# Kernel optimization log

Measured on AMD Instinct MI355X. Metric: run time of the kernel, lower is better.

## Reference

```python
import jax, jax.numpy as jnp
import numpy as np

B, N, M = 4, 512, 8192
QUERY_DIM, INPUT_DIM = 512, 256
HEADS, DIM_HEAD = 8, 64
ATT_DIM = HEADS * DIM_HEAD  # 512


def setup_inputs() -> dict:
    key = jax.random.key(0)
    ks = jax.random.split(key, 6)
    x = jax.random.normal(ks[0], (B, N, QUERY_DIM), dtype=jnp.float32)
    context = jax.random.normal(ks[1], (B, M, INPUT_DIM), dtype=jnp.float32)
    # Linear weights stored as [in, out] for x @ W
    Wq = jax.random.normal(ks[2], (QUERY_DIM, ATT_DIM), dtype=jnp.float32) / np.sqrt(QUERY_DIM)
    Wkv = jax.random.normal(ks[3], (INPUT_DIM, 2 * ATT_DIM), dtype=jnp.float32) / np.sqrt(INPUT_DIM)
    Wo = jax.random.normal(ks[4], (ATT_DIM, QUERY_DIM), dtype=jnp.float32) / np.sqrt(ATT_DIM)
    bo = jax.random.normal(ks[5], (QUERY_DIM,), dtype=jnp.float32) * 0.01
    return {"x": x, "context": context, "Wq": Wq, "Wkv": Wkv, "Wo": Wo, "bo": bo}


def reference(x, context, Wq, Wkv, Wo, bo):
    scale = DIM_HEAD ** -0.5
    q = x @ Wq                      # [B, N, H*D]
    kv = context @ Wkv              # [B, M, 2*H*D]
    k, v = jnp.split(kv, 2, axis=-1)
    # split heads: b n (h d) -> b h n d
    q = q.reshape(B, N, HEADS, DIM_HEAD).transpose(0, 2, 1, 3)
    k = k.reshape(B, M, HEADS, DIM_HEAD).transpose(0, 2, 1, 3)
    v = v.reshape(B, M, HEADS, DIM_HEAD).transpose(0, 2, 1, 3)
    scores = jnp.einsum('bhid,bhjd->bhij', q, k) * scale  # [B, H, N, M]
    attn = jax.nn.softmax(scores, axis=-1)
    out = jnp.einsum('bhij,bhjd->bhid', attn, v)           # [B, H, N, D]
    out = out.transpose(0, 2, 1, 3).reshape(B, N, ATT_DIM)
    return out @ Wo + bo
```

## Files before the change

### kernel.cpp

```cpp
#include <hip/hip_runtime.h>
#include <hip/hip_bf16.h>
#include <cstdint>

#define NB 4
#define NQ 512
#define NM 8192
#define NH 8
#define DH 64

typedef short bf16x8s __attribute__((ext_vector_type(8)));
typedef float f32x4  __attribute__((ext_vector_type(4)));

static __device__ __forceinline__ short f2bs(float f) {
    unsigned u = __builtin_bit_cast(unsigned, f);
    return (short)(unsigned short)((u + 0x8000u) >> 16);
}
static __device__ __forceinline__ unsigned pk2(float a, float b) {
    unsigned au = __builtin_bit_cast(unsigned, a) + 0x8000u;
    unsigned bu = __builtin_bit_cast(unsigned, b) + 0x8000u;
    return __builtin_amdgcn_perm(bu, au, 0x07060302u);
}

__device__ __forceinline__ void proj32_body(
    const float* __restrict__ A, const float* __restrict__ W,
    float* __restrict__ C, const float* __restrict__ bias,
    int tm, int tn, char* smemraw)
{
    short* As = (short*)smemraw;
    short* Bs = As + 32 * 72;

    const int t = threadIdx.x;
    const int w = t >> 6, ln = t & 63;
    const int m16 = ln & 15, quad = ln >> 4;
    const int wm = w >> 1, wn = w & 1;

    const int ar = t >> 3, ac = (t & 7) << 3;
    const int bn = t & 63, bkh = (t >> 6) << 4;

    const float* Ap = A + (size_t)(tm * 32 + ar) * 512 + ac;
    const float* Bp = W + (size_t)bkh * 512 + tn * 64 + bn;

    f32x4 acc[2] = {};

    for (int k0 = 0; k0 < 512; k0 += 64) {
        float4 a0 = *(const float4*)(Ap + k0);
        float4 a1 = *(const float4*)(Ap + k0 + 4);
        float bv[16];
        #pragma unroll
        for (int kk = 0; kk < 16; ++kk)
            bv[kk] = Bp[(size_t)(k0 + kk) * 512];

        __syncthreads();
        {
            uint4 wa = { pk2(a0.x,a0.y), pk2(a0.z,a0.w), pk2(a1.x,a1.y), pk2(a1.z,a1.w) };
            *(uint4*)&As[ar * 72 + ac] = wa;
            uint4 v0 = { pk2(bv[0],bv[1]),  pk2(bv[2],bv[3]),   pk2(bv[4],bv[5]),   pk2(bv[6],bv[7]) };
            uint4 v1 = { pk2(bv[8],bv[9]),  pk2(bv[10],bv[11]), pk2(bv[12],bv[13]), pk2(bv[14],bv[15]) };
            *(uint4*)&Bs[bn * 72 + bkh]     = v0;
            *(uint4*)&Bs[bn * 72 + bkh + 8] = v1;
        }
        __syncthreads();

        #pragma unroll
        for (int ks = 0; ks < 2; ++ks) {
            bf16x8s af = *(const bf16x8s*)&As[(wm * 16 + m16) * 72 + ks * 32 + quad * 8];
            #pragma unroll
            for (int nt = 0; nt < 2; ++nt) {
                bf16x8s bf = *(const bf16x8s*)&Bs[(wn * 32 + nt * 16 + m16) * 72 + ks * 32 + quad * 8];
                acc[nt] = __builtin_amdgcn_mfma_f32_16x16x32_bf16(af, bf, acc[nt], 0, 0, 0);
            }
        }
    }

    const int row0 = tm * 32 + wm * 16 + quad * 4;
    const int col0 = tn * 64 + wn * 32;
    #pragma unroll
    for (int nt = 0; nt < 2; ++nt) {
        const int col = col0 + nt * 16 + m16;
        const float bb = bias ? bias[col] : 0.f;
        #pragma unroll
        for (int r = 0; r < 4; ++r)
            C[(size_t)(row0 + r) * 512 + col] = acc[nt][r] + bb;
    }
}

__device__ __forceinline__ void kv_body(
    const float* __restrict__ A, const float* __restrict__ Bw,
    short* __restrict__ Kf, short* __restrict__ Vf,
    int bid, char* smemraw)
{
    short* As = (short*)smemraw;
    short* Bs = As + 128 * 40;

    const int t  = threadIdx.x;
    const int tm = bid & 255, tn = bid >> 8;
    const int w  = t >> 6, ln = t & 63;
    const int m16 = ln & 15, quad = ln >> 4;
    const int wm = w & 1, wn = w >> 1;

    const int ar = t >> 3;
    const int ac = (t & 7) << 2;
    const int sb_n = t & 127, sb_kh = (t >> 7) << 4;

    const float* Abase = A  + (size_t)(tm * 128 + ar) * 256 + ac;
    const float* Bbase = Bw + (size_t)sb_kh * 1024 + tn * 128 + sb_n;

    f32x4 acc[4][4] = {};

    for (int k0 = 0; k0 < 256; k0 += 32) {
        float4 av[4];
        #pragma unroll
        for (int p = 0; p < 4; ++p)
            av[p] = *(const float4*)(Abase + (size_t)p * 32 * 256 + k0);
        float bv[16];
        #pragma unroll
        for (int kk = 0; kk < 16; ++kk)
            bv[kk] = Bbase[(size_t)(k0 + kk) * 1024];

        __syncthreads();
        #pragma unroll
        for (int p = 0; p < 4; ++p) {
            uint2 wv = { pk2(av[p].x, av[p].y), pk2(av[p].z, av[p].w) };
            *(uint2*)&As[(p * 32 + ar) * 40 + ac] = wv;
        }
        {
            uint4 v0 = { pk2(bv[0],bv[1]),  pk2(bv[2],bv[3]),   pk2(bv[4],bv[5]),   pk2(bv[6],bv[7]) };
            uint4 v1 = { pk2(bv[8],bv[9]),  pk2(bv[10],bv[11]), pk2(bv[12],bv[13]), pk2(bv[14],bv[15]) };
            *(uint4*)&Bs[sb_n * 40 + sb_kh]     = v0;
            *(uint4*)&Bs[sb_n * 40 + sb_kh + 8] = v1;
        }
        __syncthreads();

        bf16x8s af[4], bfr[4];
        #pragma unroll
        for (int i = 0; i < 4; ++i)
            af[i] = *(const bf16x8s*)&As[(wm * 64 + i * 16 + m16) * 40 + quad * 8];
        #pragma unroll
        for (int j = 0; j < 4; ++j)
            bfr[j] = *(const bf16x8s*)&Bs[(wn * 64 + j * 16 + m16) * 40 + quad * 8];
        #pragma unroll
        for (int i = 0; i < 4; ++i)
            #pragma unroll
            for (int j = 0; j < 4; ++j)
                acc[i][j] = __builtin_amdgcn_mfma_f32_16x16x32_bf16(af[i], bfr[j], acc[i][j], 0, 0, 0);
    }

    const int col0 = tn * 128 + wn * 64;
    const int row0 = tm * 128 + wm * 64;
    const int b    = row0 >> 13;
    const int mr0  = row0 & (NM - 1);

    if (col0 < 512) {
        const int h = col0 >> 6;
        short* Kp = Kf + (size_t)(b * NH + h) * (NM * DH);
        #pragma unroll
        for (int i = 0; i < 4; ++i)
            #pragma unroll
            for (int j = 0; j < 4; ++j) {
                const int d = j * 16 + m16;
                #pragma unroll
                for (int r = 0; r < 4; ++r) {
                    const int key = mr0 + i * 16 + quad * 4 + r;
                    const int idx = ((key >> 4) * 2 + (d >> 5)) * 512
                                  + (((d >> 3) & 3) * 16 + (key & 15)) * 8 + (d & 7);
                    Kp[idx] = f2bs(acc[i][j][r]);
                }
            }
    } else {
        const int h = (col0 - 512) >> 6;
        short* Vp = Vf + (size_t)(b * NH + h) * (NM * DH);
        #pragma unroll
        for (int i = 0; i < 4; ++i)
            #pragma unroll
            for (int j = 0; j < 4; ++j) {
                const int key0 = mr0 + i * 16 + quad * 4;
                const int idx = (j * 256 + (key0 >> 5)) * 512
                              + ((((key0 >> 3) & 3) * 16 + m16) * 8) + (key0 & 7);
                uint2 pk;
                pk.x = pk2(acc[i][j][0], acc[i][j][1]);
                pk.y = pk2(acc[i][j][2], acc[i][j][3]);
                *(uint2*)(Vp + idx) = pk;
            }
    }
}

__global__ __launch_bounds__(256) void gemm_kvq(
    const float* __restrict__ x,   const float* __restrict__ Wq, float* __restrict__ q,
    const float* __restrict__ ctx, const float* __restrict__ Wkv,
    short* __restrict__ Kf, short* __restrict__ Vf)
{
    __shared__ __align__(16) char smem[20480];
    if (blockIdx.x < 512)
        proj32_body(x, Wq, q, nullptr, (int)(blockIdx.x >> 3), (int)(blockIdx.x & 7), smem);
    else
        kv_body(ctx, Wkv, Kf, Vf, (int)(blockIdx.x - 512), smem);
}

__global__ __launch_bounds__(256) void gemm_proj32(
    const float* __restrict__ A, const float* __restrict__ W,
    float* __restrict__ C, const float* __restrict__ bias)
{
    __shared__ __align__(16) char smem[(32 + 64) * 72 * 2];
    proj32_body(A, W, C, bias, (int)(blockIdx.x >> 3), (int)(blockIdx.x & 7), smem);
}

__global__ __launch_bounds__(256) void attn_mfma(
    const float* __restrict__ Q,
    const short* __restrict__ Kfr,
    const short* __restrict__ Vfr,
    float* __restrict__ Og)
{
    __shared__ __align__(16) float Obuf[4 * 32 * 68];
    __shared__ float lbuf[4 * 32];

    const int bid = blockIdx.x;
    const int xcd = bid & 7, grp = bid >> 3;
    const int bh  = xcd * 4 + (grp & 3);
    const int qt  = grp >> 2;
    const int b   = bh >> 3, h = bh & 7;
    const int t   = threadIdx.x;
    const int w   = t >> 6, ln = t & 63;
    const int m16 = ln & 15, quad = ln >> 4;

    const short* Kbase = Kfr + (size_t)bh * (NM * DH);
    const short* Vbase = Vfr + (size_t)bh * (NM * DH);

    bf16x8s qf[2][2];
    #pragma unroll
    for (int mt = 0; mt < 2; ++mt) {
        const float* qrow = Q + ((size_t)(b * NQ + qt * 32 + mt * 16 + m16)) * 512 + h * 64;
        #pragma unroll
        for (int ks = 0; ks < 2; ++ks) {
            float4 x0 = *(const float4*)(qrow + ks * 32 + quad * 8);
            float4 x1 = *(const float4*)(qrow + ks * 32 + quad * 8 + 4);
            uint4 pkv = { pk2(x0.x * 0.125f, x0.y * 0.125f), pk2(x0.z * 0.125f, x0.w * 0.125f),
                          pk2(x1.x * 0.125f, x1.y * 0.125f), pk2(x1.z * 0.125f, x1.w * 0.125f) };
            qf[mt][ks] = *reinterpret_cast<bf16x8s*>(&pkv);
        }
    }

    f32x4 o[2][4] = {};
    float lpr[2] = {0.f, 0.f};

    const int srcLo = (((quad << 1) & 3) << 4) + m16;
    const int srcHi = ((((quad << 1) + 1) & 3) << 4) + m16;
    const bool ktHi = quad >= 2;

    bf16x8s kf[4][2];
    {
        const int kc = w * 64;
        #pragma unroll
        for (int nt = 0; nt < 4; ++nt)
            #pragma unroll
            for (int ks = 0; ks < 2; ++ks)
                kf[nt][ks] = *(const bf16x8s*)(Kbase + ((((kc >> 4) + nt) * 2 + ks) << 9) + ln * 8);
    }

    for (int it = 0; it < 32; ++it) {
        const int kc = it * 256 + w * 64;

        bf16x8s vf[4][2];
        #pragma unroll
        for (int dt = 0; dt < 4; ++dt)
            #pragma unroll
            for (int ks = 0; ks < 2; ++ks)
                vf[dt][ks] = *(const bf16x8s*)(Vbase + ((dt * 256 + (kc >> 5) + ks) << 9) + ln * 8);

        f32x4 st[2][4] = {};
        #pragma unroll
        for (int kt = 0; kt < 4; ++kt)
            #pragma unroll
            for (int mt = 0; mt < 2; ++mt) {
                st[mt][kt] = __builtin_amdgcn_mfma_f32_16x16x32_bf16(kf[kt][0], qf[mt][0], st[mt][kt], 0, 0, 0);
                st[mt][kt] = __builtin_amdgcn_mfma_f32_16x16x32_bf16(kf[kt][1], qf[mt][1], st[mt][kt], 0, 0, 0);
            }

        if (it + 1 < 32) {
            const int kn = (it + 1) * 256 + w * 64;
            #pragma unroll
            for (int nt = 0; nt < 4; ++nt)
                #pragma unroll
                for (int ks = 0; ks < 2; ++ks)
                    kf[nt][ks] = *(const bf16x8s*)(Kbase + ((((kn >> 4) + nt) * 2 + ks) << 9) + ln * 8);
        }

        unsigned pp[2][4][2];
        #pragma unroll
        for (int mt = 0; mt < 2; ++mt)
            #pragma unroll
            for (int kt = 0; kt < 4; ++kt) {
                const float p0 = __expf(st[mt][kt][0]);
                const float p1 = __expf(st[mt][kt][1]);
                const float p2 = __expf(st[mt][kt][2]);
                const float p3 = __expf(st[mt][kt][3]);
                lpr[mt] += (p0 + p1) + (p2 + p3);
                pp[mt][kt][0] = pk2(p0, p1);
                pp[mt][kt][1] = pk2(p2, p3);
            }

        #pragma unroll
        for (int mt = 0; mt < 2; ++mt)
            #pragma unroll
            for (int ks = 0; ks < 2; ++ks) {
                const unsigned a0 = __shfl(pp[mt][2 * ks][0], srcLo);
                const unsigned b0 = __shfl(pp[mt][2 * ks + 1][0], srcLo);
                const unsigned a1 = __shfl(pp[mt][2 * ks][1], srcLo);
                const unsigned b1 = __shfl(pp[mt][2 * ks + 1][1], srcLo);
                const unsigned a2 = __shfl(pp[mt][2 * ks][0], srcHi);
                const unsigned b2 = __shfl(pp[mt][2 * ks + 1][0], srcHi);
                const unsigned a3 = __shfl(pp[mt][2 * ks][1], srcHi);
                const unsigned b3 = __shfl(pp[mt][2 * ks + 1][1], srcHi);
                uint4 pb;
                pb.x = ktHi ? b0 : a0;
                pb.y = ktHi ? b1 : a1;
                pb.z = ktHi ? b2 : a2;
                pb.w = ktHi ? b3 : a3;
                bf16x8s pbv = *reinterpret_cast<bf16x8s*>(&pb);
                #pragma unroll
                for (int dt = 0; dt < 4; ++dt)
                    o[mt][dt] = __builtin_amdgcn_mfma_f32_16x16x32_bf16(vf[dt][ks], pbv, o[mt][dt], 0, 0, 0);
            }
    }

    float lf[2];
    #pragma unroll
    for (int mt = 0; mt < 2; ++mt) {
        float l = lpr[mt];
        l += __shfl_xor(l, 16);
        l += __shfl_xor(l, 32);
        lf[mt] = l;
    }

    #pragma unroll
    for (int mt = 0; mt < 2; ++mt)
        #pragma unroll
        for (int dt = 0; dt < 4; ++dt)
            *(f32x4*)&Obuf[(w * 32 + mt * 16 + m16) * 68 + dt * 16 + quad * 4] = o[mt][dt];
    if (quad == 0) {
        lbuf[w * 32 +      m16] = lf[0];
        lbuf[w * 32 + 16 + m16] = lf[1];
    }
    __syncthreads();
    {
        const int row = t >> 3, d0 = (t & 7) << 3;
        const float l = lbuf[row] + lbuf[32 + row] + lbuf[64 + row] + lbuf[96 + row];
        const float inv = 1.0f / l;
        float res[8];
        #pragma unroll
        for (int j = 0; j < 8; ++j) {
            float a = Obuf[(row) * 68 + d0 + j]
                    + Obuf[(32 + row) * 68 + d0 + j]
                    + Obuf[(64 + row) * 68 + d0 + j]
                    + Obuf[(96 + row) * 68 + d0 + j];
            res[j] = a * inv;
        }
        float* op = Og + ((size_t)(b * NQ + qt * 32 + row)) * 512 + h * 64 + d0;
        float4 r0 = {res[0], res[1], res[2], res[3]};
        float4 r1 = {res[4], res[5], res[6], res[7]};
        *(float4*)op = r0;
        *(float4*)(op + 4) = r1;
    }
}

extern "C" void kernel_launch(void* const* d_in, const int* in_sizes, int n_in,
                              void* d_out, int out_size, void* d_ws, size_t ws_size,
                              hipStream_t stream) {
    (void)in_sizes; (void)n_in; (void)out_size; (void)ws_size;

    const float* x   = (const float*)d_in[0];
    const float* ctx = (const float*)d_in[1];
    const float* Wq  = (const float*)d_in[2];
    const float* Wkv = (const float*)d_in[3];
    const float* Wo  = (const float*)d_in[4];
    const float* bo  = (const float*)d_in[5];
    float* out = (float*)d_out;

    float* ws    = (float*)d_ws;
    float* q     = ws;
    float* attno = q + (size_t)2048 * 512;
    short* Kf    = (short*)(attno + (size_t)2048 * 512);
    short* Vf    = Kf + (size_t)NB * NH * NM * DH;

    gemm_kvq<<<dim3(2560), dim3(256), 0, stream>>>(x, Wq, q, ctx, Wkv, Kf, Vf);

    attn_mfma<<<dim3(512), dim3(256), 0, stream>>>(q, Kf, Vf, attno);

    gemm_proj32<<<dim3(512), dim3(256), 0, stream>>>(attno, Wo, out, bo);
}
```

Before: 205.3 us.

## Pre-pack weights into MFMA fragment layout and offload softmax row sums to MFMA

Adds a prep kernel that converts Wq, Wo and Wkv to bf16 in MFMA B-fragment order, so the GEMMs load B fragments straight from global memory. This removes the strided fp32 loads, LDS staging and LDS reads for weights, and halves shared memory. In attention, exp is replaced by exp2 with log2e folded into the Q scale, and the row sum is computed by an extra MFMA against a ones vector instead of VALU adds and shuffles. The cost is one extra kernel launch and weight conversion work on every call.

```diff
diff --git a/kernel.cpp b/kernel.cpp
--- a/kernel.cpp
+++ b/kernel.cpp
@@ -21,13 +21,39 @@
     return __builtin_amdgcn_perm(bu, au, 0x07060302u);
 }
 
+#if __has_builtin(__builtin_amdgcn_exp2f)
+static __device__ __forceinline__ float fexp2(float x) { return __builtin_amdgcn_exp2f(x); }
+#else
+static __device__ __forceinline__ float fexp2(float x) { return exp2f(x); }
+#endif
+
+__global__ __launch_bounds__(256) void prep_weights(
+    const float* __restrict__ Wq, const float* __restrict__ Wo,
+    const float* __restrict__ Wkv,
+    short* __restrict__ Wqf, short* __restrict__ Wof, short* __restrict__ Wkvf)
+{
+    const int t = threadIdx.x;
+    const int w = t >> 6, ln = t & 63;
+    const int m16 = ln & 15, quad = ln >> 4;
+    int f = blockIdx.x * 4 + w;
+    const float* src; short* dst; int N, KS, n0, ks;
+    if (f < 512)       { src = Wq;  dst = Wqf;  N = 512;  KS = 16; n0 = f >> 4; ks = f & 15; }
+    else if (f < 1024) { f -= 512;  src = Wo;  dst = Wof;  N = 512;  KS = 16; n0 = f >> 4; ks = f & 15; }
+    else               { f -= 1024; src = Wkv; dst = Wkvf; N = 1024; KS = 8;  n0 = f >> 3; ks = f & 7; }
+    const float* sp = src + (size_t)(ks * 32 + quad * 8) * N + n0 * 16 + m16;
+    float v[8];
+    #pragma unroll
+    for (int j = 0; j < 8; ++j) v[j] = sp[(size_t)j * N];
+    uint4 pkv = { pk2(v[0],v[1]), pk2(v[2],v[3]), pk2(v[4],v[5]), pk2(v[6],v[7]) };
+    *(uint4*)(dst + ((size_t)(n0 * KS + ks) * 64 + ln) * 8) = pkv;
+}
+
 __device__ __forceinline__ void proj32_body(
-    const float* __restrict__ A, const float* __restrict__ W,
+    const float* __restrict__ A, const short* __restrict__ Wf,
     float* __restrict__ C, const float* __restrict__ bias,
     int tm, int tn, char* smemraw)
 {
     short* As = (short*)smemraw;
-    short* Bs = As + 32 * 72;
 
     const int t = threadIdx.x;
     const int w = t >> 6, ln = t & 63;
@@ -35,29 +61,26 @@
     const int wm = w >> 1, wn = w & 1;
 
     const int ar = t >> 3, ac = (t & 7) << 3;
-    const int bn = t & 63, bkh = (t >> 6) << 4;
 
     const float* Ap = A + (size_t)(tm * 32 + ar) * 512 + ac;
-    const float* Bp = W + (size_t)bkh * 512 + tn * 64 + bn;
 
     f32x4 acc[2] = {};
 
     for (int k0 = 0; k0 < 512; k0 += 64) {
         float4 a0 = *(const float4*)(Ap + k0);
         float4 a1 = *(const float4*)(Ap + k0 + 4);
-        float bv[16];
-        #pragma unroll
-        for (int kk = 0; kk < 16; ++kk)
-            bv[kk] = Bp[(size_t)(k0 + kk) * 512];
+        bf16x8s bfr[2][2];
+        #pragma unroll
+        for (int ks = 0; ks < 2; ++ks)
+            #pragma unroll
+            for (int nt = 0; nt < 2; ++nt)
+                bfr[ks][nt] = *(const bf16x8s*)(Wf +
+                    ((size_t)((tn * 4 + wn * 2 + nt) * 16 + (k0 >> 5) + ks) * 64 + ln) * 8);
 
         __syncthreads();
         {
             uint4 wa = { pk2(a0.x,a0.y), pk2(a0.z,a0.w), pk2(a1.x,a1.y), pk2(a1.z,a1.w) };
             *(uint4*)&As[ar * 72 + ac] = wa;
-            uint4 v0 = { pk2(bv[0],bv[1]),  pk2(bv[2],bv[3]),   pk2(bv[4],bv[5]),   pk2(bv[6],bv[7]) };
-            uint4 v1 = { pk2(bv[8],bv[9]),  pk2(bv[10],bv[11]), pk2(bv[12],bv[13]), pk2(bv[14],bv[15]) };
-            *(uint4*)&Bs[bn * 72 + bkh]     = v0;
-            *(uint4*)&Bs[bn * 72 + bkh + 8] = v1;
         }
         __syncthreads();
 
@@ -65,10 +88,8 @@
         for (int ks = 0; ks < 2; ++ks) {
             bf16x8s af = *(const bf16x8s*)&As[(wm * 16 + m16) * 72 + ks * 32 + quad * 8];
             #pragma unroll
-            for (int nt = 0; nt < 2; ++nt) {
-                bf16x8s bf = *(const bf16x8s*)&Bs[(wn * 32 + nt * 16 + m16) * 72 + ks * 32 + quad * 8];
-                acc[nt] = __builtin_amdgcn_mfma_f32_16x16x32_bf16(af, bf, acc[nt], 0, 0, 0);
-            }
+            for (int nt = 0; nt < 2; ++nt)
+                acc[nt] = __builtin_amdgcn_mfma_f32_16x16x32_bf16(af, bfr[ks][nt], acc[nt], 0, 0, 0);
         }
     }
 
@@ -85,12 +106,11 @@
 }
 
 __device__ __forceinline__ void kv_body(
-    const float* __restrict__ A, const float* __restrict__ Bw,
+    const float* __restrict__ A, const short* __restrict__ Wkvf,
     short* __restrict__ Kf, short* __restrict__ Vf,
     int bid, char* smemraw)
 {
     short* As = (short*)smemraw;
-    short* Bs = As + 128 * 40;
 
     const int t  = threadIdx.x;
     const int tm = bid & 255, tn = bid >> 8;
@@ -100,10 +120,8 @@
 
     const int ar = t >> 3;
     const int ac = (t & 7) << 2;
-    const int sb_n = t & 127, sb_kh = (t >> 7) << 4;
-
-    const float* Abase = A  + (size_t)(tm * 128 + ar) * 256 + ac;
-    const float* Bbase = Bw + (size_t)sb_kh * 1024 + tn * 128 + sb_n;
+
+    const float* Abase = A + (size_t)(tm * 128 + ar) * 256 + ac;
 
     f32x4 acc[4][4] = {};
 
@@ -112,10 +130,11 @@
         #pragma unroll
         for (int p = 0; p < 4; ++p)
             av[p] = *(const float4*)(Abase + (size_t)p * 32 * 256 + k0);
-        float bv[16];
-        #pragma unroll
-        for (int kk = 0; kk < 16; ++kk)
-            bv[kk] = Bbase[(size_t)(k0 + kk) * 1024];
+        bf16x8s bfr[4];
+        #pragma unroll
+        for (int j = 0; j < 4; ++j)
+            bfr[j] = *(const bf16x8s*)(Wkvf +
+                ((size_t)((tn * 8 + wn * 4 + j) * 8 + (k0 >> 5)) * 64 + ln) * 8);
 
         __syncthreads();
         #pragma unroll
@@ -123,21 +142,12 @@
             uint2 wv = { pk2(av[p].x, av[p].y), pk2(av[p].z, av[p].w) };
             *(uint2*)&As[(p * 32 + ar) * 40 + ac] = wv;
         }
-        {
-            uint4 v0 = { pk2(bv[0],bv[1]),  pk2(bv[2],bv[3]),   pk2(bv[4],bv[5]),   pk2(bv[6],bv[7]) };
-            uint4 v1 = { pk2(bv[8],bv[9]),  pk2(bv[10],bv[11]), pk2(bv[12],bv[13]), pk2(bv[14],bv[15]) };
-            *(uint4*)&Bs[sb_n * 40 + sb_kh]     = v0;
-            *(uint4*)&Bs[sb_n * 40 + sb_kh + 8] = v1;
-        }
         __syncthreads();
 
-        bf16x8s af[4], bfr[4];
+        bf16x8s af[4];
         #pragma unroll
         for (int i = 0; i < 4; ++i)
             af[i] = *(const bf16x8s*)&As[(wm * 64 + i * 16 + m16) * 40 + quad * 8];
-        #pragma unroll
-        for (int j = 0; j < 4; ++j)
-            bfr[j] = *(const bf16x8s*)&Bs[(wn * 64 + j * 16 + m16) * 40 + quad * 8];
         #pragma unroll
         for (int i = 0; i < 4; ++i)
             #pragma unroll
@@ -185,23 +195,23 @@
 }
 
 __global__ __launch_bounds__(256) void gemm_kvq(
-    const float* __restrict__ x,   const float* __restrict__ Wq, float* __restrict__ q,
-    const float* __restrict__ ctx, const float* __restrict__ Wkv,
+    const float* __restrict__ x,   const short* __restrict__ Wqf, float* __restrict__ q,
+    const float* __restrict__ ctx, const short* __restrict__ Wkvf,
     short* __restrict__ Kf, short* __restrict__ Vf)
 {
-    __shared__ __align__(16) char smem[20480];
+    __shared__ __align__(16) char smem[10240];
     if (blockIdx.x < 512)
-        proj32_body(x, Wq, q, nullptr, (int)(blockIdx.x >> 3), (int)(blockIdx.x & 7), smem);
+        proj32_body(x, Wqf, q, nullptr, (int)(blockIdx.x >> 3), (int)(blockIdx.x & 7), smem);
     else
-        kv_body(ctx, Wkv, Kf, Vf, (int)(blockIdx.x - 512), smem);
+        kv_body(ctx, Wkvf, Kf, Vf, (int)(blockIdx.x - 512), smem);
 }
 
 __global__ __launch_bounds__(256) void gemm_proj32(
-    const float* __restrict__ A, const float* __restrict__ W,
+    const float* __restrict__ A, const short* __restrict__ Wf,
     float* __restrict__ C, const float* __restrict__ bias)
 {
-    __shared__ __align__(16) char smem[(32 + 64) * 72 * 2];
-    proj32_body(A, W, C, bias, (int)(blockIdx.x >> 3), (int)(blockIdx.x & 7), smem);
+    __shared__ __align__(16) char smem[32 * 72 * 2];
+    proj32_body(A, Wf, C, bias, (int)(blockIdx.x >> 3), (int)(blockIdx.x & 7), smem);
 }
 
 __global__ __launch_bounds__(256) void attn_mfma(
@@ -225,6 +235,7 @@
     const short* Kbase = Kfr + (size_t)bh * (NM * DH);
     const short* Vbase = Vfr + (size_t)bh * (NM * DH);
 
+    const float qsc = 0.125f * 1.44269504f;
     bf16x8s qf[2][2];
     #pragma unroll
     for (int mt = 0; mt < 2; ++mt) {
@@ -233,14 +244,18 @@
         for (int ks = 0; ks < 2; ++ks) {
             float4 x0 = *(const float4*)(qrow + ks * 32 + quad * 8);
             float4 x1 = *(const float4*)(qrow + ks * 32 + quad * 8 + 4);
-            uint4 pkv = { pk2(x0.x * 0.125f, x0.y * 0.125f), pk2(x0.z * 0.125f, x0.w * 0.125f),
-                          pk2(x1.x * 0.125f, x1.y * 0.125f), pk2(x1.z * 0.125f, x1.w * 0.125f) };
+            uint4 pkv = { pk2(x0.x * qsc, x0.y * qsc), pk2(x0.z * qsc, x0.w * qsc),
+                          pk2(x1.x * qsc, x1.y * qsc), pk2(x1.z * qsc, x1.w * qsc) };
             qf[mt][ks] = *reinterpret_cast<bf16x8s*>(&pkv);
         }
     }
 
+    bf16x8s ones;
+    #pragma unroll
+    for (int j = 0; j < 8; ++j) ones[j] = (short)0x3F80;
+
     f32x4 o[2][4] = {};
-    float lpr[2] = {0.f, 0.f};
+    f32x4 lsum[2] = {};
 
     const int srcLo = (((quad << 1) & 3) << 4) + m16;
     const int srcHi = ((((quad << 1) + 1) & 3) << 4) + m16;
@@ -289,11 +304,10 @@
         for (int mt = 0; mt < 2; ++mt)
             #pragma unroll
             for (int kt = 0; kt < 4; ++kt) {
-                const float p0 = __expf(st[mt][kt][0]);
-                const float p1 = __expf(st[mt][kt][1]);
-                const float p2 = __expf(st[mt][kt][2]);
-                const float p3 = __expf(st[mt][kt][3]);
-                lpr[mt] += (p0 + p1) + (p2 + p3);
+                const float p0 = fexp2(st[mt][kt][0]);
+                const float p1 = fexp2(st[mt][kt][1]);
+                const float p2 = fexp2(st[mt][kt][2]);
+                const float p3 = fexp2(st[mt][kt][3]);
                 pp[mt][kt][0] = pk2(p0, p1);
                 pp[mt][kt][1] = pk2(p2, p3);
             }
@@ -319,16 +333,8 @@
                 #pragma unroll
                 for (int dt = 0; dt < 4; ++dt)
                     o[mt][dt] = __builtin_amdgcn_mfma_f32_16x16x32_bf16(vf[dt][ks], pbv, o[mt][dt], 0, 0, 0);
+                lsum[mt] = __builtin_amdgcn_mfma_f32_16x16x32_bf16(ones, pbv, lsum[mt], 0, 0, 0);
             }
-    }
-
-    float lf[2];
-    #pragma unroll
-    for (int mt = 0; mt < 2; ++mt) {
-        float l = lpr[mt];
-        l += __shfl_xor(l, 16);
-        l += __shfl_xor(l, 32);
-        lf[mt] = l;
     }
 
     #pragma unroll
@@ -337,8 +343,8 @@
         for (int dt = 0; dt < 4; ++dt)
             *(f32x4*)&Obuf[(w * 32 + mt * 16 + m16) * 68 + dt * 16 + quad * 4] = o[mt][dt];
     if (quad == 0) {
-        lbuf[w * 32 +      m16] = lf[0];
-        lbuf[w * 32 + 16 + m16] = lf[1];
+        lbuf[w * 32 +      m16] = lsum[0][0];
+        lbuf[w * 32 + 16 + m16] = lsum[1][0];
     }
     __syncthreads();
     {
@@ -380,10 +386,15 @@
     float* attno = q + (size_t)2048 * 512;
     short* Kf    = (short*)(attno + (size_t)2048 * 512);
     short* Vf    = Kf + (size_t)NB * NH * NM * DH;
-
-    gemm_kvq<<<dim3(2560), dim3(256), 0, stream>>>(x, Wq, q, ctx, Wkv, Kf, Vf);
+    short* Wqf   = Vf + (size_t)NB * NH * NM * DH;
+    short* Wof   = Wqf + (size_t)512 * 512;
+    short* Wkvf  = Wof + (size_t)512 * 512;
+
+    prep_weights<<<dim3(384), dim3(256), 0, stream>>>(Wq, Wo, Wkv, Wqf, Wof, Wkvf);
+
+    gemm_kvq<<<dim3(2560), dim3(256), 0, stream>>>(x, Wqf, q, ctx, Wkvf, Kf, Vf);
 
     attn_mfma<<<dim3(512), dim3(256), 0, stream>>>(q, Kf, Vf, attno);
 
-    gemm_proj32<<<dim3(512), dim3(256), 0, stream>>>(attno, Wo, out, bo);
-}
+    gemm_proj32<<<dim3(512), dim3(256), 0, stream>>>(attno, Wof, out, bo);
+}
```

Result: faster. 191.9 us (-6.5%).
